# Performance work log

Measured on AMD Instinct MI355X. Metric: run time of the kernel, lower is better.

The kernel has to match this reference:

```python
import jax, jax.numpy as jnp
import numpy as np

B, S, D, H = 2, 2048, 1024, 16
DK = D // H


def setup_inputs() -> dict:
    key = jax.random.key(0)
    ks = jax.random.split(key, 10)
    scale = 1.0 / np.sqrt(D)
    x = jax.random.normal(ks[0], (B, S, D), dtype=jnp.float32)
    # causal mask: 1 = attend, 0 = masked (module's create_causal_mask)
    mask = jnp.tril(jnp.ones((S, S), dtype=jnp.int32))[None, None]
    Wq = jax.random.normal(ks[1], (D, D), jnp.float32) * scale
    bq = jax.random.normal(ks[2], (D,), jnp.float32) * 0.01
    Wk = jax.random.normal(ks[3], (D, D), jnp.float32) * scale
    bk = jax.random.normal(ks[4], (D,), jnp.float32) * 0.01
    Wv = jax.random.normal(ks[5], (D, D), jnp.float32) * scale
    bv = jax.random.normal(ks[6], (D,), jnp.float32) * 0.01
    Wo = jax.random.normal(ks[7], (D, D), jnp.float32) * scale
    bo = jax.random.normal(ks[8], (D,), jnp.float32) * 0.01
    return {"x": x, "mask": mask, "Wq": Wq, "bq": bq, "Wk": Wk, "bk": bk,
            "Wv": Wv, "bv": bv, "Wo": Wo, "bo": bo}


def reference(x, mask, Wq, bq, Wk, bk, Wv, bv, Wo, bo):
    b, s, _ = x.shape
    # projections; [B,S,D] -> [B,H,S,DK]
    def split_heads(t):
        return t.reshape(b, s, H, DK).transpose(0, 2, 1, 3)
    Q = split_heads(x @ Wq + bq)
    K = split_heads(x @ Wk + bk)
    V = split_heads(x @ Wv + bv)
    scores = jnp.einsum('bhqd,bhkd->bhqk', Q, K) / np.sqrt(DK)
    scores = jnp.where(mask == 0, jnp.float32(-1e9), scores)
    attn = jax.nn.softmax(scores, axis=-1)  # dropout p=0 -> identity
    ctx = jnp.einsum('bhqk,bhkd->bhqd', attn, V)
    ctx = ctx.transpose(0, 2, 1, 3).reshape(b, s, D)
    return ctx @ Wo + bo
```

## Files before the change

### kernel.cpp

```cpp
#include <hip/hip_runtime.h>
#include <hip/hip_bf16.h>


typedef _Float16 f16x8 __attribute__((ext_vector_type(8)));
typedef _Float16 f16x4 __attribute__((ext_vector_type(4)));
typedef float f32x4 __attribute__((ext_vector_type(4)));

#define QSCALE 0.180336880111112f

__device__ __forceinline__ void async_copy16(const _Float16* gsrc,
                                             _Float16* ldst) {
  __builtin_amdgcn_global_load_lds(
      (const __attribute__((address_space(1))) void*)gsrc,
      (__attribute__((address_space(3))) void*)ldst, 16, 0, 0);
}

__global__ __launch_bounds__(256) void cvt_x(const float* __restrict__ x,
                                             _Float16* __restrict__ xh) {
  int i = (blockIdx.x * 256 + threadIdx.x) * 4;
  float4 v = *(const float4*)(x + i);
  f16x4 o;
  o.x = (_Float16)v.x; o.y = (_Float16)v.y;
  o.z = (_Float16)v.z; o.w = (_Float16)v.w;
  *(f16x4*)(xh + i) = o;
}

__global__ __launch_bounds__(256) void wt_kernel(
    const float* __restrict__ W0, const float* __restrict__ W1,
    const float* __restrict__ W2, const float* __restrict__ W3,
    _Float16* __restrict__ T0, _Float16* __restrict__ T1,
    _Float16* __restrict__ T2, _Float16* __restrict__ T3) {
  const float* W; _Float16* T;
  switch (blockIdx.z) {
    case 0: W = W0; T = T0; break;
    case 1: W = W1; T = T1; break;
    case 2: W = W2; T = T2; break;
    default: W = W3; T = T3; break;
  }
  __shared__ _Float16 tile[32][33];
  const int tx = threadIdx.x & 31, ty = threadIdx.x >> 5;
  const int n0 = blockIdx.x * 32, k0 = blockIdx.y * 32;
  for (int i = 0; i < 4; i++) {
    int kk = k0 + ty + i * 8;
    tile[ty + i * 8][tx] = (_Float16)W[(size_t)kk * 1024 + n0 + tx];
  }
  __syncthreads();
  for (int i = 0; i < 4; i++) {
    int nn = n0 + ty + i * 8;
    T[(size_t)nn * 1024 + k0 + tx] = tile[tx][ty + i * 8];
  }
}

__global__ __launch_bounds__(256) void gemm_qkv(
    const _Float16* __restrict__ A, const _Float16* __restrict__ BtAll,
    const float* __restrict__ bq, const float* __restrict__ bk,
    const float* __restrict__ bv, _Float16* __restrict__ Qh,
    _Float16* __restrict__ Kh, _Float16* __restrict__ VT) {
  __shared__ _Float16 As[128 * 32];
  __shared__ _Float16 Bs[128 * 32];
  const int tid = threadIdx.x;
  const int wave = tid >> 6, lane = tid & 63;
  const int lr = lane & 15, lq = lane >> 4;
  const int m0 = blockIdx.x * 128, n0 = blockIdx.y * 128;
  const int rw = (wave & 1) * 64, cw = (wave >> 1) * 64;

  const int sel = blockIdx.y >> 3;
  const float* bias = sel == 0 ? bq : (sel == 1 ? bk : bv);
  const int c0 = n0 & 1023;

  f32x4 acc[4][4] = {};
  const int r0 = wave * 32 + (lane >> 2);
  const int woff = (lane & 3) * 8;

  for (int kt = 0; kt < 1024; kt += 32) {
    __syncthreads();
    async_copy16(A + (size_t)(m0 + r0) * 1024 + kt + woff, As + r0 * 32 + woff);
    async_copy16(A + (size_t)(m0 + r0 + 16) * 1024 + kt + woff,
                 As + (r0 + 16) * 32 + woff);
    async_copy16(BtAll + (size_t)(n0 + r0) * 1024 + kt + woff,
                 Bs + r0 * 32 + woff);
    async_copy16(BtAll + (size_t)(n0 + r0 + 16) * 1024 + kt + woff,
                 Bs + (r0 + 16) * 32 + woff);
    __syncthreads();
    f16x8 af[4], bf[4];
    for (int i = 0; i < 4; i++)
      af[i] = *(const f16x8*)(As + (rw + i * 16 + lr) * 32 + lq * 8);
    for (int j = 0; j < 4; j++)
      bf[j] = *(const f16x8*)(Bs + (cw + j * 16 + lr) * 32 + lq * 8);
    for (int i = 0; i < 4; i++)
      for (int j = 0; j < 4; j++)
        acc[i][j] = __builtin_amdgcn_mfma_f32_16x16x32_f16(af[i], bf[j],
                                                           acc[i][j], 0, 0, 0);
  }

  if (sel == 2) {
    for (int i = 0; i < 4; i++) {
      const int row = m0 + rw + i * 16 + lq * 4;
      const int bb = row >> 11, ss = row & 2047;
      for (int j = 0; j < 4; j++) {
        const int col = c0 + cw + j * 16 + lr;
        const int hh = col >> 6, dk = col & 63;
        const float bvl = bias[col];
        f16x4 pv;
        for (int r = 0; r < 4; r++) pv[r] = (_Float16)(acc[i][j][r] + bvl);
        *(f16x4*)(VT + ((size_t)(bb * 16 + hh) * 64 + dk) * 2048 + ss) = pv;
      }
    }
  } else {
    _Float16* out = sel == 0 ? Qh : Kh;
    const float scl = sel == 0 ? QSCALE : 1.0f;
    for (int i = 0; i < 4; i++) {
      const int row = m0 + rw + i * 16 + lq * 4;
      for (int j = 0; j < 4; j++) {
        const int col = c0 + cw + j * 16 + lr;
        const float bvl = bias[col];
        for (int r = 0; r < 4; r++)
          out[(size_t)(row + r) * 1024 + col] =
              (_Float16)((acc[i][j][r] + bvl) * scl);
      }
    }
  }
}

__global__ __launch_bounds__(256) void gemm_out(
    const _Float16* __restrict__ A, const _Float16* __restrict__ Bt,
    const float* __restrict__ bias, float* __restrict__ out) {
  __shared__ _Float16 As[128 * 32];
  __shared__ _Float16 Bs[128 * 32];
  const int tid = threadIdx.x;
  const int wave = tid >> 6, lane = tid & 63;
  const int lr = lane & 15, lq = lane >> 4;
  const int m0 = blockIdx.x * 128, n0 = blockIdx.y * 128;
  const int rw = (wave & 1) * 64, cw = (wave >> 1) * 64;
  f32x4 acc[4][4] = {};
  const int r0 = wave * 32 + (lane >> 2);
  const int woff = (lane & 3) * 8;

  for (int kt = 0; kt < 1024; kt += 32) {
    __syncthreads();
    async_copy16(A + (size_t)(m0 + r0) * 1024 + kt + woff, As + r0 * 32 + woff);
    async_copy16(A + (size_t)(m0 + r0 + 16) * 1024 + kt + woff,
                 As + (r0 + 16) * 32 + woff);
    async_copy16(Bt + (size_t)(n0 + r0) * 1024 + kt + woff,
                 Bs + r0 * 32 + woff);
    async_copy16(Bt + (size_t)(n0 + r0 + 16) * 1024 + kt + woff,
                 Bs + (r0 + 16) * 32 + woff);
    __syncthreads();
    f16x8 af[4], bf[4];
    for (int i = 0; i < 4; i++)
      af[i] = *(const f16x8*)(As + (rw + i * 16 + lr) * 32 + lq * 8);
    for (int j = 0; j < 4; j++)
      bf[j] = *(const f16x8*)(Bs + (cw + j * 16 + lr) * 32 + lq * 8);
    for (int i = 0; i < 4; i++)
      for (int j = 0; j < 4; j++)
        acc[i][j] = __builtin_amdgcn_mfma_f32_16x16x32_f16(af[i], bf[j],
                                                           acc[i][j], 0, 0, 0);
  }
  for (int i = 0; i < 4; i++) {
    const int row = m0 + rw + i * 16 + lq * 4;
    for (int j = 0; j < 4; j++) {
      const int col = n0 + cw + j * 16 + lr;
      const float bvl = bias[col];
      for (int r = 0; r < 4; r++)
        out[(size_t)(row + r) * 1024 + col] = acc[i][j][r] + bvl;
    }
  }
}

__global__ __launch_bounds__(256) void attn(const _Float16* __restrict__ Q,
                                            const _Float16* __restrict__ K,
                                            const _Float16* __restrict__ VT,
                                            _Float16* __restrict__ ctx) {
  const int j = blockIdx.x;
  const int h = blockIdx.y, b = blockIdx.z;
  const int tid = threadIdx.x, wave = tid >> 6, lane = tid & 63;
  const int lr = lane & 15, lq = lane >> 4;
  const size_t qkbase = ((size_t)b * 2048) * 1024 + h * 64;
  const size_t vtbase = ((size_t)(b * 16 + h)) * 64 * 2048;

  __shared__ _Float16 Ks[2][64 * 72];
  __shared__ _Float16 Vs[2][64 * 72];

  const int sgr = tid >> 2, sgc = (tid & 3) * 8;
  const _Float16* Kg0 = K + qkbase + (size_t)sgr * 1024 + sgc;
  const _Float16* Vg0 = VT + vtbase + (size_t)sgr * 2048 + sgc;

  for (int phase = 0; phase < 2; phase++) {
    const int qt = phase ? (31 - j) : j;
    const int q0 = qt * 64;
    const _Float16* qp =
        Q + qkbase + (size_t)(q0 + wave * 16 + lr) * 1024 + lq * 8;
    f16x8 qf0 = *(const f16x8*)qp;
    f16x8 qf1 = *(const f16x8*)(qp + 32);

    float mrow = -1e30f, lsum = 0.f;
    f32x4 o[4] = {};

    uint4 ka = *(const uint4*)Kg0, kb = *(const uint4*)(Kg0 + 32);
    uint4 va = *(const uint4*)Vg0, vb = *(const uint4*)(Vg0 + 32);
    __syncthreads();

    for (int t = 0; t <= qt; t++) {
      _Float16* ksb = Ks[t & 1];
      _Float16* vsb = Vs[t & 1];
      *(uint4*)(ksb + sgr * 72 + sgc) = ka;
      *(uint4*)(ksb + sgr * 72 + sgc + 32) = kb;
      *(uint4*)(vsb + sgr * 72 + sgc) = va;
      *(uint4*)(vsb + sgr * 72 + sgc + 32) = vb;
      __syncthreads();
      if (t < qt) {
        const _Float16* kg = Kg0 + (size_t)(t + 1) * 64 * 1024;
        const _Float16* vg = Vg0 + (t + 1) * 64;
        ka = *(const uint4*)kg; kb = *(const uint4*)(kg + 32);
        va = *(const uint4*)vg; vb = *(const uint4*)(vg + 32);
      }

      f32x4 s[4];
      for (int ks = 0; ks < 4; ks++) {
        f16x8 k0 = *(const f16x8*)(ksb + (ks * 16 + lr) * 72 + lq * 8);
        f16x8 k1 = *(const f16x8*)(ksb + (ks * 16 + lr) * 72 + 32 + lq * 8);
        f32x4 z = {};
        z = __builtin_amdgcn_mfma_f32_16x16x32_f16(k0, qf0, z, 0, 0, 0);
        z = __builtin_amdgcn_mfma_f32_16x16x32_f16(k1, qf1, z, 0, 0, 0);
        s[ks] = z;
      }
      if (t == qt) {
        const int qcol = q0 + wave * 16 + lr;
        const int kv0 = t * 64;
        for (int ks = 0; ks < 4; ks++)
          for (int r = 0; r < 4; r++)
            if (kv0 + ks * 16 + lq * 4 + r > qcol) s[ks][r] = -1e30f;
      }
      float mx = s[0][0];
      for (int ks = 0; ks < 4; ks++)
        for (int r = 0; r < 4; r++) mx = fmaxf(mx, s[ks][r]);
      mx = fmaxf(mx, __shfl_xor(mx, 16));
      mx = fmaxf(mx, __shfl_xor(mx, 32));
      float mnew = fmaxf(mrow, mx);
      float alpha = exp2f(mrow - mnew);
      mrow = mnew;
      float rs = 0.f;
      f16x4 pa[4];
      for (int ks = 0; ks < 4; ks++)
        for (int r = 0; r < 4; r++) {
          float p = exp2f(s[ks][r] - mnew);
          rs += p;
          pa[ks][r] = (_Float16)p;
        }
      rs += __shfl_xor(rs, 16);
      rs += __shfl_xor(rs, 32);
      lsum = lsum * alpha + rs;
      float ar[4];
      for (int r = 0; r < 4; r++) ar[r] = __shfl(alpha, lq * 4 + r);
      for (int dn = 0; dn < 4; dn++)
        for (int r = 0; r < 4; r++) o[dn][r] *= ar[r];
      for (int ks = 0; ks < 4; ks++)
        for (int dn = 0; dn < 4; dn++) {
          f16x4 vf = *(const f16x4*)(vsb + (dn * 16 + lr) * 72 + ks * 16 + lq * 4);
          o[dn] =
              __builtin_amdgcn_mfma_f32_16x16x16f16(pa[ks], vf, o[dn], 0, 0, 0);
        }
    }

    for (int r = 0; r < 4; r++) {
      float lv = __shfl(lsum, lq * 4 + r);
      float inv = 1.0f / lv;
      const int row = q0 + wave * 16 + lq * 4 + r;
      for (int dn = 0; dn < 4; dn++)
        ctx[qkbase + (size_t)row * 1024 + dn * 16 + lr] =
            (_Float16)(o[dn][r] * inv);
    }
  }
}

extern "C" void kernel_launch(void* const* d_in, const int* in_sizes, int n_in,
                              void* d_out, int out_size, void* d_ws,
                              size_t ws_size, hipStream_t stream) {
  const float* x  = (const float*)d_in[0];
  const float* Wq = (const float*)d_in[2];
  const float* bq = (const float*)d_in[3];
  const float* Wk = (const float*)d_in[4];
  const float* bk = (const float*)d_in[5];
  const float* Wv = (const float*)d_in[6];
  const float* bv = (const float*)d_in[7];
  const float* Wo = (const float*)d_in[8];
  const float* bo = (const float*)d_in[9];
  float* out = (float*)d_out;

  char* ws = (char*)d_ws;
  const size_t MB = 1 << 20;
  _Float16* xh  = (_Float16*)(ws);
  _Float16* WTs = (_Float16*)(ws + 8 * MB);
  _Float16* WqT = WTs;
  _Float16* WkT = (_Float16*)(ws + 10 * MB);
  _Float16* WvT = (_Float16*)(ws + 12 * MB);
  _Float16* WoT = (_Float16*)(ws + 14 * MB);
  _Float16* Qh  = (_Float16*)(ws + 16 * MB);
  _Float16* Kh  = (_Float16*)(ws + 24 * MB);
  _Float16* VT  = (_Float16*)(ws + 32 * MB);
  _Float16* ctx = (_Float16*)(ws);

  cvt_x<<<4096, 256, 0, stream>>>(x, xh);
  wt_kernel<<<dim3(32, 32, 4), 256, 0, stream>>>(Wq, Wk, Wv, Wo, WqT, WkT, WvT,
                                                 WoT);
  gemm_qkv<<<dim3(32, 24), 256, 0, stream>>>(xh, WTs, bq, bk, bv, Qh, Kh, VT);
  attn<<<dim3(16, 16, 2), 256, 0, stream>>>(Qh, Kh, VT, ctx);
  gemm_out<<<dim3(32, 8), 256, 0, stream>>>(ctx, WoT, bo, out);
}
```

Baseline: 210.5 us.

## Fuse prep kernels and restructure attention into 128-row, 8-wave blocks

Merges the x conversion and weight transpose into one launch to cut a kernel launch. Reworks attention so each 512-thread block handles one 128-row query tile with 8 waves sharing the K/V LDS tiles, instead of 4 waves processing a paired short and long tile in two phases. Heaviest tiles are scheduled first, waves skip fully masked KV tiles, and the rescale of the output accumulator is skipped when the running max is unchanged. Trades the old balanced pairing for larger blocks, which may cause wave imbalance within a block and lower occupancy.

Result: slower. 234.3 us (+11.3%).

```diff
diff --git a/kernel.cpp b/kernel.cpp
--- a/kernel.cpp
+++ b/kernel.cpp
@@ -15,23 +15,26 @@
       (__attribute__((address_space(3))) void*)ldst, 16, 0, 0);
 }
 
-__global__ __launch_bounds__(256) void cvt_x(const float* __restrict__ x,
-                                             _Float16* __restrict__ xh) {
-  int i = (blockIdx.x * 256 + threadIdx.x) * 4;
-  float4 v = *(const float4*)(x + i);
-  f16x4 o;
-  o.x = (_Float16)v.x; o.y = (_Float16)v.y;
-  o.z = (_Float16)v.z; o.w = (_Float16)v.w;
-  *(f16x4*)(xh + i) = o;
-}
-
-__global__ __launch_bounds__(256) void wt_kernel(
+__global__ __launch_bounds__(256) void prep(
+    const float* __restrict__ x, _Float16* __restrict__ xh,
     const float* __restrict__ W0, const float* __restrict__ W1,
     const float* __restrict__ W2, const float* __restrict__ W3,
     _Float16* __restrict__ T0, _Float16* __restrict__ T1,
     _Float16* __restrict__ T2, _Float16* __restrict__ T3) {
+  if (blockIdx.x < 4096) {
+    int i = (blockIdx.x * 256 + threadIdx.x) * 4;
+    float4 v = *(const float4*)(x + i);
+    f16x4 o;
+    o.x = (_Float16)v.x; o.y = (_Float16)v.y;
+    o.z = (_Float16)v.z; o.w = (_Float16)v.w;
+    *(f16x4*)(xh + i) = o;
+    return;
+  }
+  const int id = blockIdx.x - 4096;
+  const int w = id >> 10, rem = id & 1023;
+  const int bx = rem & 31, by = rem >> 5;
   const float* W; _Float16* T;
-  switch (blockIdx.z) {
+  switch (w) {
     case 0: W = W0; T = T0; break;
     case 1: W = W1; T = T1; break;
     case 2: W = W2; T = T2; break;
@@ -39,7 +42,7 @@
   }
   __shared__ _Float16 tile[32][33];
   const int tx = threadIdx.x & 31, ty = threadIdx.x >> 5;
-  const int n0 = blockIdx.x * 32, k0 = blockIdx.y * 32;
+  const int n0 = bx * 32, k0 = by * 32;
   for (int i = 0; i < 4; i++) {
     int kk = k0 + ty + i * 8;
     tile[ty + i * 8][tx] = (_Float16)W[(size_t)kk * 1024 + n0 + tx];
@@ -167,54 +170,49 @@
   }
 }
 
-__global__ __launch_bounds__(256) void attn(const _Float16* __restrict__ Q,
+__global__ __launch_bounds__(512) void attn(const _Float16* __restrict__ Q,
                                             const _Float16* __restrict__ K,
                                             const _Float16* __restrict__ VT,
                                             _Float16* __restrict__ ctx) {
-  const int j = blockIdx.x;
+  const int qt = 15 - blockIdx.x;
   const int h = blockIdx.y, b = blockIdx.z;
   const int tid = threadIdx.x, wave = tid >> 6, lane = tid & 63;
   const int lr = lane & 15, lq = lane >> 4;
+  const int q0 = qt * 128;
+  const int qmin = q0 + wave * 16;
   const size_t qkbase = ((size_t)b * 2048) * 1024 + h * 64;
   const size_t vtbase = ((size_t)(b * 16 + h)) * 64 * 2048;
 
   __shared__ _Float16 Ks[2][64 * 72];
   __shared__ _Float16 Vs[2][64 * 72];
 
-  const int sgr = tid >> 2, sgc = (tid & 3) * 8;
+  const _Float16* qp = Q + qkbase + (size_t)(qmin + lr) * 1024 + lq * 8;
+  f16x8 qf0 = *(const f16x8*)qp;
+  f16x8 qf1 = *(const f16x8*)(qp + 32);
+
+  float mrow = -1e30f, lsum = 0.f;
+  f32x4 o[4] = {};
+
+  const int sgr = tid >> 3, sgc = (tid & 7) * 8;
   const _Float16* Kg0 = K + qkbase + (size_t)sgr * 1024 + sgc;
   const _Float16* Vg0 = VT + vtbase + (size_t)sgr * 2048 + sgc;
-
-  for (int phase = 0; phase < 2; phase++) {
-    const int qt = phase ? (31 - j) : j;
-    const int q0 = qt * 64;
-    const _Float16* qp =
-        Q + qkbase + (size_t)(q0 + wave * 16 + lr) * 1024 + lq * 8;
-    f16x8 qf0 = *(const f16x8*)qp;
-    f16x8 qf1 = *(const f16x8*)(qp + 32);
-
-    float mrow = -1e30f, lsum = 0.f;
-    f32x4 o[4] = {};
-
-    uint4 ka = *(const uint4*)Kg0, kb = *(const uint4*)(Kg0 + 32);
-    uint4 va = *(const uint4*)Vg0, vb = *(const uint4*)(Vg0 + 32);
-    __syncthreads();
-
-    for (int t = 0; t <= qt; t++) {
-      _Float16* ksb = Ks[t & 1];
-      _Float16* vsb = Vs[t & 1];
-      *(uint4*)(ksb + sgr * 72 + sgc) = ka;
-      *(uint4*)(ksb + sgr * 72 + sgc + 32) = kb;
-      *(uint4*)(vsb + sgr * 72 + sgc) = va;
-      *(uint4*)(vsb + sgr * 72 + sgc + 32) = vb;
-      __syncthreads();
-      if (t < qt) {
-        const _Float16* kg = Kg0 + (size_t)(t + 1) * 64 * 1024;
-        const _Float16* vg = Vg0 + (t + 1) * 64;
-        ka = *(const uint4*)kg; kb = *(const uint4*)(kg + 32);
-        va = *(const uint4*)vg; vb = *(const uint4*)(vg + 32);
-      }
-
+  uint4 ka = *(const uint4*)Kg0;
+  uint4 va = *(const uint4*)Vg0;
+
+  const int tmax = 2 * qt + 1;
+  for (int t = 0;; t++) {
+    _Float16* ksb = Ks[t & 1];
+    _Float16* vsb = Vs[t & 1];
+    *(uint4*)(ksb + sgr * 72 + sgc) = ka;
+    *(uint4*)(vsb + sgr * 72 + sgc) = va;
+    __syncthreads();
+    if (t < tmax) {
+      ka = *(const uint4*)(Kg0 + (size_t)(t + 1) * 64 * 1024);
+      va = *(const uint4*)(Vg0 + (t + 1) * 64);
+    }
+
+    const int kv0 = t * 64;
+    if (kv0 <= qmin + 15) {
       f32x4 s[4];
       for (int ks = 0; ks < 4; ks++) {
         f16x8 k0 = *(const f16x8*)(ksb + (ks * 16 + lr) * 72 + lq * 8);
@@ -224,9 +222,8 @@
         z = __builtin_amdgcn_mfma_f32_16x16x32_f16(k1, qf1, z, 0, 0, 0);
         s[ks] = z;
       }
-      if (t == qt) {
-        const int qcol = q0 + wave * 16 + lr;
-        const int kv0 = t * 64;
+      if (kv0 + 63 > qmin) {
+        const int qcol = qmin + lr;
         for (int ks = 0; ks < 4; ks++)
           for (int r = 0; r < 4; r++)
             if (kv0 + ks * 16 + lq * 4 + r > qcol) s[ks][r] = -1e30f;
@@ -250,26 +247,30 @@
       rs += __shfl_xor(rs, 16);
       rs += __shfl_xor(rs, 32);
       lsum = lsum * alpha + rs;
-      float ar[4];
-      for (int r = 0; r < 4; r++) ar[r] = __shfl(alpha, lq * 4 + r);
-      for (int dn = 0; dn < 4; dn++)
-        for (int r = 0; r < 4; r++) o[dn][r] *= ar[r];
+      if (__any(alpha != 1.0f)) {
+        float ar[4];
+        for (int r = 0; r < 4; r++) ar[r] = __shfl(alpha, lq * 4 + r);
+        for (int dn = 0; dn < 4; dn++)
+          for (int r = 0; r < 4; r++) o[dn][r] *= ar[r];
+      }
       for (int ks = 0; ks < 4; ks++)
         for (int dn = 0; dn < 4; dn++) {
-          f16x4 vf = *(const f16x4*)(vsb + (dn * 16 + lr) * 72 + ks * 16 + lq * 4);
+          f16x4 vf =
+              *(const f16x4*)(vsb + (dn * 16 + lr) * 72 + ks * 16 + lq * 4);
           o[dn] =
               __builtin_amdgcn_mfma_f32_16x16x16f16(pa[ks], vf, o[dn], 0, 0, 0);
         }
     }
-
-    for (int r = 0; r < 4; r++) {
-      float lv = __shfl(lsum, lq * 4 + r);
-      float inv = 1.0f / lv;
-      const int row = q0 + wave * 16 + lq * 4 + r;
-      for (int dn = 0; dn < 4; dn++)
-        ctx[qkbase + (size_t)row * 1024 + dn * 16 + lr] =
-            (_Float16)(o[dn][r] * inv);
-    }
+    if (t == tmax) break;
+  }
+
+  for (int r = 0; r < 4; r++) {
+    float lv = __shfl(lsum, lq * 4 + r);
+    float inv = 1.0f / lv;
+    const int row = qmin + lq * 4 + r;
+    for (int dn = 0; dn < 4; dn++)
+      ctx[qkbase + (size_t)row * 1024 + dn * 16 + lr] =
+          (_Float16)(o[dn][r] * inv);
   }
 }
 
@@ -300,10 +301,8 @@
   _Float16* VT  = (_Float16*)(ws + 32 * MB);
   _Float16* ctx = (_Float16*)(ws);
 
-  cvt_x<<<4096, 256, 0, stream>>>(x, xh);
-  wt_kernel<<<dim3(32, 32, 4), 256, 0, stream>>>(Wq, Wk, Wv, Wo, WqT, WkT, WvT,
-                                                 WoT);
+  prep<<<8192, 256, 0, stream>>>(x, xh, Wq, Wk, Wv, Wo, WqT, WkT, WvT, WoT);
   gemm_qkv<<<dim3(32, 24), 256, 0, stream>>>(xh, WTs, bq, bk, bv, Qh, Kh, VT);
-  attn<<<dim3(16, 16, 2), 256, 0, stream>>>(Qh, Kh, VT, ctx);
+  attn<<<dim3(16, 16, 2), 512, 0, stream>>>(Qh, Kh, VT, ctx);
   gemm_out<<<dim3(32, 8), 256, 0, stream>>>(ctx, WoT, bo, out);
 }
```
